# Optimization experiments

Hardware: AMD Instinct MI355X
Metric: run time of the kernel (lower is better)

Reference implementation:

```python
import jax, jax.numpy as jnp
import numpy as np

DIM = 1024
HEADS = 16
HEAD_DIM = DIM // HEADS
B, NQ, NK = 2, 2048, 2048


def setup_inputs() -> dict:
    key = jax.random.key(0)
    ks = jax.random.split(key, 8)
    s = 1.0 / np.sqrt(DIM)
    return {
        "query": jax.random.normal(ks[0], (B, NQ, DIM), jnp.float32),
        "key": jax.random.normal(ks[1], (B, NK, DIM), jnp.float32),
        "value": jax.random.normal(ks[2], (B, NK, DIM), jnp.float32),
        "qpos": jnp.zeros((B, NQ), jnp.int32),
        "kpos": jnp.zeros((B, NK), jnp.int32),
        "Wq": jax.random.normal(ks[3], (DIM, DIM), jnp.float32) * s,
        "Wk": jax.random.normal(ks[4], (DIM, DIM), jnp.float32) * s,
        "Wv": jax.random.normal(ks[5], (DIM, DIM), jnp.float32) * s,
        "Wo": jax.random.normal(ks[6], (DIM, DIM), jnp.float32) * s,
        "bo": jax.random.normal(ks[7], (DIM,), jnp.float32) * s,
    }


def reference(query, key, value, qpos, kpos, Wq, Wk, Wv, Wo, bo):
    # torch nn.Linear: y = x @ W.T (qkv_bias=False)
    Bq, Nq, C = query.shape
    Nk = key.shape[1]
    scale = HEAD_DIM ** -0.5
    # project and split heads: (B, H, N, Dh)
    q = (query @ Wq.T).reshape(Bq, Nq, HEADS, HEAD_DIM).transpose(0, 2, 1, 3)
    k = (key @ Wk.T).reshape(Bq, Nk, HEADS, HEAD_DIM).transpose(0, 2, 1, 3)
    v = (value @ Wv.T).reshape(Bq, Nk, HEADS, HEAD_DIM).transpose(0, 2, 1, 3)
    # rope is None, qk_norm False -> plain softmax attention
    attn = jnp.einsum("bhqd,bhkd->bhqk", q, k) * scale  # [B,H,Nq,Nk]
    attn = jax.nn.softmax(attn, axis=-1)
    x = jnp.einsum("bhqk,bhkd->bhqd", attn, v)
    x = x.transpose(0, 2, 1, 3).reshape(Bq, Nq, C)
    return x @ Wo.T + bo
```

## Files before the change

### kernel.cpp

```cpp
#include <hip/hip_runtime.h>
#include <hip/hip_bf16.h>
#include <stdint.h>

typedef __bf16 bf16_t;
typedef __bf16 bf16x4 __attribute__((ext_vector_type(4)));
typedef __bf16 bf16x8 __attribute__((ext_vector_type(8)));
typedef float  f32x4  __attribute__((ext_vector_type(4)));
typedef unsigned u32x2 __attribute__((ext_vector_type(2)));

#define MFMA16(a,b,c) __builtin_amdgcn_mfma_f32_16x16x32_bf16((a),(b),(c),0,0,0)

static constexpr int DIM = 1024, HEADS = 16, HD = 64, NB = 2, NQ = 2048, NKK = 2048;
static constexpr int MROWS = NB * NQ;
static constexpr float SCALE_Q = 0.18033688011112042f;

__global__ void cvt_w(const float* __restrict__ wq, const float* __restrict__ wk,
                      const float* __restrict__ wv, const float* __restrict__ wo,
                      bf16_t* wqb, bf16_t* wkb, bf16_t* wvb, bf16_t* wob) {
  const int t = blockIdx.y;
  const float* src = t == 0 ? wq : t == 1 ? wk : t == 2 ? wv : wo;
  bf16_t* dst = t == 0 ? wqb : t == 1 ? wkb : t == 2 ? wvb : wob;
  size_t i = (size_t)blockIdx.x * 256 + threadIdx.x;
  float4 val = reinterpret_cast<const float4*>(src)[i];
  bf16x4 o;
  o[0] = (bf16_t)val.x; o[1] = (bf16_t)val.y; o[2] = (bf16_t)val.z; o[3] = (bf16_t)val.w;
  *reinterpret_cast<bf16x4*>(dst + i * 4) = o;
}

template<int ROWS, int TPB = 256>
__device__ __forceinline__ void stage_swz(const bf16_t* gbase, int gstride, bf16_t* lds, int tid) {
#pragma unroll
  for (int c = 0; c < ROWS * 8 / TPB; ++c) {
    int p = c * TPB + tid;
    int r = p >> 3, x = p & 7;
    const bf16_t* src = gbase + (size_t)r * gstride + ((x ^ (r & 7)) << 3);
    __builtin_amdgcn_global_load_lds(
        (const __attribute__((address_space(1))) void*)src,
        (__attribute__((address_space(3))) void*)(lds + (p << 3)),
        16, 0, 0);
  }
}

__device__ __forceinline__ void stage_f32(const float* gbase, int gstride, bf16_t* lds, int tid) {
#pragma unroll
  for (int c = 0; c < 4; ++c) {
    int p = c * 256 + tid;
    int r = p >> 3, x = p & 7;
    const float* src = gbase + (size_t)r * gstride + ((x ^ (r & 7)) << 3);
    float4 a = *reinterpret_cast<const float4*>(src);
    float4 b2 = *reinterpret_cast<const float4*>(src + 4);
    bf16x8 o;
    o[0] = (bf16_t)a.x;  o[1] = (bf16_t)a.y;  o[2] = (bf16_t)a.z;  o[3] = (bf16_t)a.w;
    o[4] = (bf16_t)b2.x; o[5] = (bf16_t)b2.y; o[6] = (bf16_t)b2.z; o[7] = (bf16_t)b2.w;
    *reinterpret_cast<bf16x8*>(lds + (p << 3)) = o;
  }
}

__device__ __forceinline__ bf16x8 lds_read8_swz(const bf16_t* lds, int row, int chunk) {
  int sc = chunk ^ (row & 7);
  return *reinterpret_cast<const bf16x8*>(lds + row * 64 + (sc << 3));
}

__device__ __forceinline__ unsigned cvtpk_bf16(float lo, float hi) {
  unsigned r;
  asm("v_cvt_pk_bf16_f32 %0, %1, %2" : "=v"(r) : "v"(lo), "v"(hi));
  return r;
}

__global__ __launch_bounds__(256) void gemm_qkv(const float* __restrict__ qf32,
                                                const float* __restrict__ kf32,
                                                const float* __restrict__ vf32,
                                                const bf16_t* __restrict__ Wq,
                                                const bf16_t* __restrict__ Wk,
                                                const bf16_t* __restrict__ Wv,
                                                bf16_t* __restrict__ Qp,
                                                bf16_t* __restrict__ Kp,
                                                bf16_t* __restrict__ Vt) {
  constexpr int K = DIM, N = DIM;
  __shared__ __align__(16) bf16_t As[128 * 64];
  __shared__ __align__(16) bf16_t Bs[128 * 64];
  const int tid = threadIdx.x;
  const int lane = tid & 63, wid = tid >> 6;
  const int l15 = lane & 15, lg = lane >> 4;
  const int wr = wid >> 1, wc = wid & 1;

  int d = blockIdx.x + 24 * blockIdx.y;
  int j = d & 7, rest = d >> 3;
  int m_ = rest & 7, gq = rest >> 3;
  int g = 8 * gq + j;
  const int bm = g / 3, sel = g % 3, bnl = m_;

  const float*  Af = sel == 0 ? qf32 : sel == 1 ? kf32 : vf32;
  const bf16_t* Bt = sel == 0 ? Wq : sel == 1 ? Wk : Wv;
  const float*  Abase = Af + (size_t)(bm * 128) * K;
  const bf16_t* Bbase = Bt + (size_t)(bnl * 128) * K;

  f32x4 acc[4][4];
#pragma unroll
  for (int m = 0; m < 4; ++m)
#pragma unroll
    for (int n = 0; n < 4; ++n) acc[m][n] = (f32x4){0.f, 0.f, 0.f, 0.f};

  for (int k0 = 0; k0 < K; k0 += 64) {
    __syncthreads();
    stage_f32(Abase + k0, K, As, tid);
    stage_swz<128>(Bbase + k0, K, Bs, tid);
    __syncthreads();
#pragma unroll
    for (int kk = 0; kk < 2; ++kk) {
      bf16x8 af[4], bfr[4];
#pragma unroll
      for (int m = 0; m < 4; ++m) af[m] = lds_read8_swz(As, wr * 64 + m * 16 + l15, kk * 4 + lg);
#pragma unroll
      for (int n = 0; n < 4; ++n) bfr[n] = lds_read8_swz(Bs, wc * 64 + n * 16 + l15, kk * 4 + lg);
#pragma unroll
      for (int m = 0; m < 4; ++m)
#pragma unroll
        for (int n = 0; n < 4; ++n)
          acc[m][n] = MFMA16(af[m], bfr[n], acc[m][n]);
    }
  }

  if (sel == 2) {
#pragma unroll
    for (int m = 0; m < 4; ++m) {
      int row0 = bm * 128 + wr * 64 + m * 16 + lg * 4;
      int bb = row0 >> 11, kv = row0 & 2047;
#pragma unroll
      for (int n = 0; n < 4; ++n) {
        int col = bnl * 128 + wc * 64 + n * 16 + l15;
        int hh = col >> 6, dd = col & 63;
        bf16x4 pk;
#pragma unroll
        for (int jj = 0; jj < 4; ++jj) pk[jj] = (bf16_t)acc[m][n][jj];
        *reinterpret_cast<bf16x4*>(Vt + (((size_t)((bb * 16 + hh) * 64 + dd)) << 11) + kv) = pk;
      }
    }
  } else {
    bf16_t* Cout = sel == 0 ? Qp : Kp;
    const float scale = sel == 0 ? SCALE_Q : 1.0f;
#pragma unroll
    for (int m = 0; m < 4; ++m)
#pragma unroll
      for (int n = 0; n < 4; ++n)
#pragma unroll
        for (int jj = 0; jj < 4; ++jj) {
          int row = bm * 128 + wr * 64 + m * 16 + lg * 4 + jj;
          int col = bnl * 128 + wc * 64 + n * 16 + l15;
          Cout[(size_t)row * N + col] = (bf16_t)(acc[m][n][jj] * scale);
        }
  }
}

__global__ __launch_bounds__(256) void gemm_out(const bf16_t* __restrict__ A,
                                                const bf16_t* __restrict__ Bt,
                                                float* __restrict__ Cout,
                                                const float* __restrict__ bias) {
  constexpr int K = DIM, N = DIM;
  __shared__ __align__(16) bf16_t As[128 * 64];
  __shared__ __align__(16) bf16_t Bs[128 * 64];
  const int tid = threadIdx.x;
  const int lane = tid & 63, wid = tid >> 6;
  const int l15 = lane & 15, lg = lane >> 4;
  const int wr = wid >> 1, wc = wid & 1;
  const int bn = blockIdx.x, bm = blockIdx.y;

  const bf16_t* Abase = A + (size_t)(bm * 128) * K;
  const bf16_t* Bbase = Bt + (size_t)(bn * 128) * K;

  f32x4 acc[4][4];
#pragma unroll
  for (int m = 0; m < 4; ++m)
#pragma unroll
    for (int n = 0; n < 4; ++n) acc[m][n] = (f32x4){0.f, 0.f, 0.f, 0.f};

  for (int k0 = 0; k0 < K; k0 += 64) {
    __syncthreads();
    stage_swz<128>(Abase + k0, K, As, tid);
    stage_swz<128>(Bbase + k0, K, Bs, tid);
    __syncthreads();
#pragma unroll
    for (int kk = 0; kk < 2; ++kk) {
      bf16x8 af[4], bfr[4];
#pragma unroll
      for (int m = 0; m < 4; ++m) af[m] = lds_read8_swz(As, wr * 64 + m * 16 + l15, kk * 4 + lg);
#pragma unroll
      for (int n = 0; n < 4; ++n) bfr[n] = lds_read8_swz(Bs, wc * 64 + n * 16 + l15, kk * 4 + lg);
#pragma unroll
      for (int m = 0; m < 4; ++m)
#pragma unroll
        for (int n = 0; n < 4; ++n)
          acc[m][n] = MFMA16(af[m], bfr[n], acc[m][n]);
    }
  }

#pragma unroll
  for (int m = 0; m < 4; ++m)
#pragma unroll
    for (int n = 0; n < 4; ++n)
#pragma unroll
      for (int j = 0; j < 4; ++j) {
        int row = bm * 128 + wr * 64 + m * 16 + lg * 4 + j;
        int col = bn * 128 + wc * 64 + n * 16 + l15;
        Cout[(size_t)row * N + col] = acc[m][n][j] + bias[col];
      }
}

__global__ __launch_bounds__(512) void attn_fused(const bf16_t* __restrict__ Qp,
                                                  const bf16_t* __restrict__ Kp,
                                                  const bf16_t* __restrict__ Vt,
                                                  bf16_t* __restrict__ Xa) {
  __shared__ __align__(16) bf16_t Ks[4][64 * 64];
  __shared__ __align__(16) bf16_t Vs[4][64 * 64];
  __shared__ __align__(16) bf16_t Ps[8][16 * 64];
  const int tid = threadIdx.x;
  const int lane = tid & 63, wid = tid >> 6;
  const int l15 = lane & 15, lg = lane >> 4;
  const int rot = (l15 & 7) * 8;

  int id = blockIdx.x + 16 * (blockIdx.y + 16 * blockIdx.z);
  int swz = (id & 7) * 64 + (id >> 3);
  const int bx = swz & 15, h = (swz >> 4) & 15, b = swz >> 8;
  const int q0 = bx * 128;

  const bf16_t* qbase = Qp + ((size_t)(b * NQ + q0)) * DIM + h * HD;
  const bf16_t* kbase = Kp + ((size_t)b * NKK) * DIM + h * HD;
  const bf16_t* vbase = Vt + ((size_t)((b * HEADS + h) * HD)) * NKK;

  stage_swz<128, 512>(qbase, DIM, &Ks[0][0], tid);
  __syncthreads();
  bf16x8 qf[2];
  qf[0] = lds_read8_swz(&Ks[0][0], wid * 16 + l15, lg);
  qf[1] = lds_read8_swz(&Ks[0][0], wid * 16 + l15, 4 + lg);
  __syncthreads();

  float m_ = -1e30f, l_ = 0.f;
  f32x4 o[4];
#pragma unroll
  for (int n = 0; n < 4; ++n) o[n] = (f32x4){0.f, 0.f, 0.f, 0.f};

  constexpr int NT = NKK / 64;

  stage_swz<64, 512>(kbase, DIM, &Ks[0][0], tid);
  stage_swz<64, 512>(vbase, NKK, &Vs[0][0], tid);
  stage_swz<64, 512>(kbase + (size_t)64 * DIM, DIM, &Ks[1][0], tid);
  stage_swz<64, 512>(vbase + 64, NKK, &Vs[1][0], tid);

  for (int t = 0; t < NT; t += 2) {
    if (t + 2 < NT) {
      stage_swz<64, 512>(kbase + (size_t)(t + 2) * 64 * DIM, DIM, &Ks[(t + 2) & 3][0], tid);
      stage_swz<64, 512>(vbase + (t + 2) * 64, NKK, &Vs[(t + 2) & 3][0], tid);
      stage_swz<64, 512>(kbase + (size_t)(t + 3) * 64 * DIM, DIM, &Ks[(t + 3) & 3][0], tid);
      stage_swz<64, 512>(vbase + (t + 3) * 64, NKK, &Vs[(t + 3) & 3][0], tid);
      asm volatile("s_waitcnt vmcnt(4)" ::: "memory");
    } else {
      asm volatile("s_waitcnt vmcnt(0)" ::: "memory");
    }
    __builtin_amdgcn_s_barrier();
    __builtin_amdgcn_sched_barrier(0);

#pragma unroll
    for (int u = 0; u < 2; ++u) {
      const int j = t + u;
      const bf16_t* kl = &Ks[j & 3][0];
      const bf16_t* vl = &Vs[j & 3][0];

      f32x4 scur[4];
      __builtin_amdgcn_s_setprio(1);
#pragma unroll
      for (int tt = 0; tt < 4; ++tt) {
        bf16x8 kf0 = lds_read8_swz(kl, tt * 16 + l15, lg);
        bf16x8 kf1 = lds_read8_swz(kl, tt * 16 + l15, 4 + lg);
        f32x4 a = (f32x4){0.f, 0.f, 0.f, 0.f};
        a = MFMA16(kf0, qf[0], a);
        a = MFMA16(kf1, qf[1], a);
        scur[tt] = a;
      }
      __builtin_amdgcn_s_setprio(0);

      float rm = scur[0][0];
#pragma unroll
      for (int tt = 0; tt < 4; ++tt)
#pragma unroll
        for (int jj = 0; jj < 4; ++jj) rm = fmaxf(rm, scur[tt][jj]);
      rm = fmaxf(rm, __shfl_xor(rm, 16));
      rm = fmaxf(rm, __shfl_xor(rm, 32));
      if (!__all(rm <= m_ + 8.f)) {
        float mn = fmaxf(m_, rm);
        float al = exp2f(m_ - mn);
        m_ = mn;
        l_ *= al;
#pragma unroll
        for (int n = 0; n < 4; ++n)
#pragma unroll
          for (int jj = 0; jj < 4; ++jj) o[n][jj] *= al;
      }
      float rs = 0.f;
#pragma unroll
      for (int tt = 0; tt < 4; ++tt)
#pragma unroll
        for (int jj = 0; jj < 4; ++jj) {
          float p = exp2f(scur[tt][jj] - m_);
          scur[tt][jj] = p;
          rs += p;
        }
      rs += __shfl_xor(rs, 16);
      rs += __shfl_xor(rs, 32);
      l_ += rs;

      bf16_t* Pw = &Ps[wid][0];
#pragma unroll
      for (int tt = 0; tt < 4; ++tt) {
        unsigned w0 = cvtpk_bf16(scur[tt][0], scur[tt][1]);
        unsigned w1 = cvtpk_bf16(scur[tt][2], scur[tt][3]);
        int col = (16 * tt + 4 * lg + rot) & 63;
        u32x2 pk2 = {w0, w1};
        *reinterpret_cast<u32x2*>(reinterpret_cast<char*>(Pw) + l15 * 128 + col * 2) = pk2;
      }
      asm volatile("s_waitcnt lgkmcnt(0)" ::: "memory");
      bf16x8 pf[2];
#pragma unroll
      for (int kt = 0; kt < 2; ++kt) {
        int col = (32 * kt + 8 * lg + rot) & 63;
        pf[kt] = *reinterpret_cast<const bf16x8*>(reinterpret_cast<const char*>(Pw) + l15 * 128 + col * 2);
      }

      __builtin_amdgcn_s_setprio(1);
#pragma unroll
      for (int n = 0; n < 4; ++n) {
#pragma unroll
        for (int kt = 0; kt < 2; ++kt) {
          bf16x8 vf = lds_read8_swz(vl, n * 16 + l15, 4 * kt + lg);
          o[n] = MFMA16(vf, pf[kt], o[n]);
        }
      }
      __builtin_amdgcn_s_setprio(0);
    }

    __builtin_amdgcn_s_barrier();
    __builtin_amdgcn_sched_barrier(0);
  }

  float inv = 1.f / l_;
  int q = q0 + wid * 16 + l15;
  bf16_t* ob = Xa + ((size_t)(b * NQ + q)) * DIM + h * HD;
#pragma unroll
  for (int n = 0; n < 4; ++n) {
    bf16x4 pk;
#pragma unroll
    for (int j = 0; j < 4; ++j) pk[j] = (bf16_t)(o[n][j] * inv);
    *reinterpret_cast<bf16x4*>(ob + n * 16 + 4 * lg) = pk;
  }
}

extern "C" void kernel_launch(void* const* d_in, const int* in_sizes, int n_in,
                              void* d_out, int out_size, void* d_ws, size_t ws_size,
                              hipStream_t stream) {
  (void)in_sizes; (void)n_in; (void)out_size; (void)ws_size;
  const float* q  = (const float*)d_in[0];
  const float* k  = (const float*)d_in[1];
  const float* v  = (const float*)d_in[2];
  const float* Wq = (const float*)d_in[5];
  const float* Wk = (const float*)d_in[6];
  const float* Wv = (const float*)d_in[7];
  const float* Wo = (const float*)d_in[8];
  const float* bo = (const float*)d_in[9];
  float* out = (float*)d_out;

  bf16_t* ws = (bf16_t*)d_ws;
  const size_t SZ_IN = (size_t)MROWS * DIM;
  const size_t SZ_W  = (size_t)DIM * DIM;
  bf16_t* qb  = ws;
  bf16_t* kb  = qb  + SZ_IN;
  bf16_t* vb  = kb  + SZ_IN;
  bf16_t* wqb = vb  + SZ_IN;
  bf16_t* wkb = wqb + SZ_W;
  bf16_t* wvb = wkb + SZ_W;
  bf16_t* wob = wvb + SZ_W;
  bf16_t* Qp  = wob + SZ_W;
  bf16_t* Kp  = Qp  + SZ_IN;
  bf16_t* Vtp = Kp  + SZ_IN;
  bf16_t* Xa  = qb;

  cvt_w<<<dim3(1024, 4), 256, 0, stream>>>(Wq, Wk, Wv, Wo, wqb, wkb, wvb, wob);

  gemm_qkv<<<dim3(24, MROWS / 128), 256, 0, stream>>>(q, k, v, wqb, wkb, wvb,
                                                      Qp, Kp, Vtp);

  attn_fused<<<dim3(NQ / 128, HEADS, NB), 512, 0, stream>>>(Qp, Kp, Vtp, Xa);

  gemm_out<<<dim3(DIM / 128, MROWS / 128), 256, 0, stream>>>(Xa, wob, out, bo);
}
```

Measured before the change: 151.6 us.

## Software-pipeline QKV GEMM with register-prefetched A and double-buffered B tiles

Restructures the QKV projection GEMM main loop so the next K-tile's fp32 A data is loaded into registers and its bf16 B tile is staged asynchronously into a second LDS buffer while the current tile is being computed. The loop is manually unrolled by two with even and odd register sets, and uses raw s_barrier plus sched_barrier instead of __syncthreads. The aim is to hide global-memory latency behind MFMA work. In exchange it adds LDS for the second B buffer and extra registers for the prefetched A rows, which may reduce occupancy. It also relies on implicit vmcnt ordering for B readiness.

Result: slower. 160.5 us (+5.9%).

```diff
diff --git a/kernel.cpp b/kernel.cpp
--- a/kernel.cpp
+++ b/kernel.cpp
@@ -41,14 +41,21 @@
   }
 }
 
-__device__ __forceinline__ void stage_f32(const float* gbase, int gstride, bf16_t* lds, int tid) {
+__device__ __forceinline__ void loadA_f32(const float* gbase, int tid, float4* r) {
 #pragma unroll
   for (int c = 0; c < 4; ++c) {
     int p = c * 256 + tid;
-    int r = p >> 3, x = p & 7;
-    const float* src = gbase + (size_t)r * gstride + ((x ^ (r & 7)) << 3);
-    float4 a = *reinterpret_cast<const float4*>(src);
-    float4 b2 = *reinterpret_cast<const float4*>(src + 4);
+    int rr = p >> 3, x = p & 7;
+    const float* src = gbase + (size_t)rr * DIM + ((x ^ (rr & 7)) << 3);
+    r[2 * c]     = *reinterpret_cast<const float4*>(src);
+    r[2 * c + 1] = *reinterpret_cast<const float4*>(src + 4);
+  }
+}
+__device__ __forceinline__ void writeA(bf16_t* lds, int tid, const float4* r) {
+#pragma unroll
+  for (int c = 0; c < 4; ++c) {
+    int p = c * 256 + tid;
+    float4 a = r[2 * c], b2 = r[2 * c + 1];
     bf16x8 o;
     o[0] = (bf16_t)a.x;  o[1] = (bf16_t)a.y;  o[2] = (bf16_t)a.z;  o[3] = (bf16_t)a.w;
     o[4] = (bf16_t)b2.x; o[5] = (bf16_t)b2.y; o[6] = (bf16_t)b2.z; o[7] = (bf16_t)b2.w;
@@ -76,9 +83,9 @@
                                                 bf16_t* __restrict__ Qp,
                                                 bf16_t* __restrict__ Kp,
                                                 bf16_t* __restrict__ Vt) {
-  constexpr int K = DIM, N = DIM;
+  constexpr int K = DIM, N = DIM, NKI = K / 64;
   __shared__ __align__(16) bf16_t As[128 * 64];
-  __shared__ __align__(16) bf16_t Bs[128 * 64];
+  __shared__ __align__(16) bf16_t Bs[2][128 * 64];
   const int tid = threadIdx.x;
   const int lane = tid & 63, wid = tid >> 6;
   const int l15 = lane & 15, lg = lane >> 4;
@@ -101,25 +108,59 @@
 #pragma unroll
     for (int n = 0; n < 4; ++n) acc[m][n] = (f32x4){0.f, 0.f, 0.f, 0.f};
 
-  for (int k0 = 0; k0 < K; k0 += 64) {
-    __syncthreads();
-    stage_f32(Abase + k0, K, As, tid);
-    stage_swz<128>(Bbase + k0, K, Bs, tid);
-    __syncthreads();
-#pragma unroll
-    for (int kk = 0; kk < 2; ++kk) {
-      bf16x8 af[4], bfr[4];
-#pragma unroll
-      for (int m = 0; m < 4; ++m) af[m] = lds_read8_swz(As, wr * 64 + m * 16 + l15, kk * 4 + lg);
-#pragma unroll
-      for (int n = 0; n < 4; ++n) bfr[n] = lds_read8_swz(Bs, wc * 64 + n * 16 + l15, kk * 4 + lg);
-#pragma unroll
-      for (int m = 0; m < 4; ++m)
-#pragma unroll
-        for (int n = 0; n < 4; ++n)
-          acc[m][n] = MFMA16(af[m], bfr[n], acc[m][n]);
-    }
-  }
+  float4 rE[8], rO[8];
+
+#define QKV_COMPUTE(BSEL)                                                      \
+  do {                                                                         \
+    _Pragma("unroll")                                                          \
+    for (int kk = 0; kk < 2; ++kk) {                                           \
+      bf16x8 af[4], bfr[4];                                                    \
+      _Pragma("unroll")                                                        \
+      for (int m = 0; m < 4; ++m)                                              \
+        af[m] = lds_read8_swz(As, wr * 64 + m * 16 + l15, kk * 4 + lg);        \
+      _Pragma("unroll")                                                        \
+      for (int n = 0; n < 4; ++n)                                              \
+        bfr[n] = lds_read8_swz(&Bs[BSEL][0], wc * 64 + n * 16 + l15, kk * 4 + lg); \
+      _Pragma("unroll")                                                        \
+      for (int m = 0; m < 4; ++m)                                              \
+        _Pragma("unroll")                                                      \
+        for (int n = 0; n < 4; ++n)                                            \
+          acc[m][n] = MFMA16(af[m], bfr[n], acc[m][n]);                        \
+    }                                                                          \
+  } while (0)
+
+  stage_swz<128>(Bbase, K, &Bs[0][0], tid);
+  loadA_f32(Abase, tid, rE);
+
+#pragma unroll 1
+  for (int t = 0; t < NKI; t += 2) {
+    __builtin_amdgcn_s_barrier();
+    __builtin_amdgcn_sched_barrier(0);
+    if (t + 1 < NKI) {
+      stage_swz<128>(Bbase + (t + 1) * 64, K, &Bs[(t + 1) & 1][0], tid);
+      loadA_f32(Abase + (t + 1) * 64, tid, rO);
+    }
+    writeA(As, tid, rE);
+    asm volatile("s_waitcnt lgkmcnt(0)" ::: "memory");
+    __builtin_amdgcn_s_barrier();
+    __builtin_amdgcn_sched_barrier(0);
+    QKV_COMPUTE(t & 1);
+
+    if (t + 1 < NKI) {
+      __builtin_amdgcn_s_barrier();
+      __builtin_amdgcn_sched_barrier(0);
+      if (t + 2 < NKI) {
+        stage_swz<128>(Bbase + (t + 2) * 64, K, &Bs[t & 1][0], tid);
+        loadA_f32(Abase + (t + 2) * 64, tid, rE);
+      }
+      writeA(As, tid, rO);
+      asm volatile("s_waitcnt lgkmcnt(0)" ::: "memory");
+      __builtin_amdgcn_s_barrier();
+      __builtin_amdgcn_sched_barrier(0);
+      QKV_COMPUTE((t + 1) & 1);
+    }
+  }
+#undef QKV_COMPUTE
 
   if (sel == 2) {
 #pragma unroll
```

## Process two 16-row query groups per wave in fused attention

Applied to the files above, without the earlier changes.

Each wave now handles 32 query rows, as two groups, instead of 16, and each block covers 256 queries instead of 128. K and V fragments are read from LDS once per tile and reused across both groups' MFMAs. The aim is to halve LDS reads and global K/V staging per query. In exchange the grid is halved to 256 blocks, and LDS and register use per block grow, so occupancy and latency hiding drop.

New measurement: 162.6 us. 1.07x slower.

```diff
diff --git a/kernel.cpp b/kernel.cpp
--- a/kernel.cpp
+++ b/kernel.cpp
@@ -212,32 +212,37 @@
                                                   bf16_t* __restrict__ Xa) {
   __shared__ __align__(16) bf16_t Ks[4][64 * 64];
   __shared__ __align__(16) bf16_t Vs[4][64 * 64];
-  __shared__ __align__(16) bf16_t Ps[8][16 * 64];
+  __shared__ __align__(16) bf16_t Ps[8][32 * 64];
   const int tid = threadIdx.x;
   const int lane = tid & 63, wid = tid >> 6;
   const int l15 = lane & 15, lg = lane >> 4;
   const int rot = (l15 & 7) * 8;
 
-  int id = blockIdx.x + 16 * (blockIdx.y + 16 * blockIdx.z);
-  int swz = (id & 7) * 64 + (id >> 3);
-  const int bx = swz & 15, h = (swz >> 4) & 15, b = swz >> 8;
-  const int q0 = bx * 128;
+  int id = blockIdx.x + 8 * (blockIdx.y + 16 * blockIdx.z);
+  int swz = (id & 7) * 32 + (id >> 3);
+  const int bx = swz & 7, h = (swz >> 3) & 15, b = swz >> 7;
+  const int q0 = bx * 256;
 
   const bf16_t* qbase = Qp + ((size_t)(b * NQ + q0)) * DIM + h * HD;
   const bf16_t* kbase = Kp + ((size_t)b * NKK) * DIM + h * HD;
   const bf16_t* vbase = Vt + ((size_t)((b * HEADS + h) * HD)) * NKK;
 
-  stage_swz<128, 512>(qbase, DIM, &Ks[0][0], tid);
+  stage_swz<256, 512>(qbase, DIM, &Ks[0][0], tid);
   __syncthreads();
-  bf16x8 qf[2];
-  qf[0] = lds_read8_swz(&Ks[0][0], wid * 16 + l15, lg);
-  qf[1] = lds_read8_swz(&Ks[0][0], wid * 16 + l15, 4 + lg);
+  bf16x8 qf[2][2];
+#pragma unroll
+  for (int g = 0; g < 2; ++g) {
+    qf[g][0] = lds_read8_swz(&Ks[0][0], wid * 32 + g * 16 + l15, lg);
+    qf[g][1] = lds_read8_swz(&Ks[0][0], wid * 32 + g * 16 + l15, 4 + lg);
+  }
   __syncthreads();
 
-  float m_ = -1e30f, l_ = 0.f;
-  f32x4 o[4];
-#pragma unroll
-  for (int n = 0; n < 4; ++n) o[n] = (f32x4){0.f, 0.f, 0.f, 0.f};
+  float m_[2] = {-1e30f, -1e30f}, l_[2] = {0.f, 0.f};
+  f32x4 o[2][4];
+#pragma unroll
+  for (int g = 0; g < 2; ++g)
+#pragma unroll
+    for (int n = 0; n < 4; ++n) o[g][n] = (f32x4){0.f, 0.f, 0.f, 0.f};
 
   constexpr int NT = NKK / 64;
 
@@ -265,91 +270,113 @@
       const bf16_t* kl = &Ks[j & 3][0];
       const bf16_t* vl = &Vs[j & 3][0];
 
-      f32x4 scur[4];
+      bf16x8 kf0[4], kf1[4];
+#pragma unroll
+      for (int tt = 0; tt < 4; ++tt) {
+        kf0[tt] = lds_read8_swz(kl, tt * 16 + l15, lg);
+        kf1[tt] = lds_read8_swz(kl, tt * 16 + l15, 4 + lg);
+      }
+
+      f32x4 s[2][4];
+#pragma unroll
+      for (int g = 0; g < 2; ++g)
+#pragma unroll
+        for (int tt = 0; tt < 4; ++tt) s[g][tt] = (f32x4){0.f, 0.f, 0.f, 0.f};
       __builtin_amdgcn_s_setprio(1);
 #pragma unroll
-      for (int tt = 0; tt < 4; ++tt) {
-        bf16x8 kf0 = lds_read8_swz(kl, tt * 16 + l15, lg);
-        bf16x8 kf1 = lds_read8_swz(kl, tt * 16 + l15, 4 + lg);
-        f32x4 a = (f32x4){0.f, 0.f, 0.f, 0.f};
-        a = MFMA16(kf0, qf[0], a);
-        a = MFMA16(kf1, qf[1], a);
-        scur[tt] = a;
+      for (int g = 0; g < 2; ++g)
+#pragma unroll
+        for (int tt = 0; tt < 4; ++tt) {
+          s[g][tt] = MFMA16(kf0[tt], qf[g][0], s[g][tt]);
+          s[g][tt] = MFMA16(kf1[tt], qf[g][1], s[g][tt]);
+        }
+      __builtin_amdgcn_s_setprio(0);
+
+#pragma unroll
+      for (int g = 0; g < 2; ++g) {
+        float rm = s[g][0][0];
+#pragma unroll
+        for (int tt = 0; tt < 4; ++tt)
+#pragma unroll
+          for (int jj = 0; jj < 4; ++jj) rm = fmaxf(rm, s[g][tt][jj]);
+        rm = fmaxf(rm, __shfl_xor(rm, 16));
+        rm = fmaxf(rm, __shfl_xor(rm, 32));
+        if (!__all(rm <= m_[g] + 8.f)) {
+          float mn = fmaxf(m_[g], rm);
+          float al = exp2f(m_[g] - mn);
+          m_[g] = mn;
+          l_[g] *= al;
+#pragma unroll
+          for (int n = 0; n < 4; ++n)
+#pragma unroll
+            for (int jj = 0; jj < 4; ++jj) o[g][n][jj] *= al;
+        }
+        float rs = 0.f;
+#pragma unroll
+        for (int tt = 0; tt < 4; ++tt)
+#pragma unroll
+          for (int jj = 0; jj < 4; ++jj) {
+            float p = exp2f(s[g][tt][jj] - m_[g]);
+            s[g][tt][jj] = p;
+            rs += p;
+          }
+        rs += __shfl_xor(rs, 16);
+        rs += __shfl_xor(rs, 32);
+        l_[g] += rs;
+      }
+
+      bf16_t* Pw = &Ps[wid][0];
+#pragma unroll
+      for (int g = 0; g < 2; ++g)
+#pragma unroll
+        for (int tt = 0; tt < 4; ++tt) {
+          unsigned w0 = cvtpk_bf16(s[g][tt][0], s[g][tt][1]);
+          unsigned w1 = cvtpk_bf16(s[g][tt][2], s[g][tt][3]);
+          int col = (16 * tt + 4 * lg + rot) & 63;
+          u32x2 pk2 = {w0, w1};
+          *reinterpret_cast<u32x2*>(reinterpret_cast<char*>(Pw) + (g * 16 + l15) * 128 + col * 2) = pk2;
+        }
+      asm volatile("s_waitcnt lgkmcnt(0)" ::: "memory");
+      bf16x8 pf[2][2];
+#pragma unroll
+      for (int g = 0; g < 2; ++g)
+#pragma unroll
+        for (int kt = 0; kt < 2; ++kt) {
+          int col = (32 * kt + 8 * lg + rot) & 63;
+          pf[g][kt] = *reinterpret_cast<const bf16x8*>(
+              reinterpret_cast<const char*>(Pw) + (g * 16 + l15) * 128 + col * 2);
+        }
+
+      __builtin_amdgcn_s_setprio(1);
+#pragma unroll
+      for (int n = 0; n < 4; ++n) {
+        bf16x8 vf0 = lds_read8_swz(vl, n * 16 + l15, lg);
+        bf16x8 vf1 = lds_read8_swz(vl, n * 16 + l15, 4 + lg);
+#pragma unroll
+        for (int g = 0; g < 2; ++g) {
+          o[g][n] = MFMA16(vf0, pf[g][0], o[g][n]);
+          o[g][n] = MFMA16(vf1, pf[g][1], o[g][n]);
+        }
       }
       __builtin_amdgcn_s_setprio(0);
-
-      float rm = scur[0][0];
-#pragma unroll
-      for (int tt = 0; tt < 4; ++tt)
-#pragma unroll
-        for (int jj = 0; jj < 4; ++jj) rm = fmaxf(rm, scur[tt][jj]);
-      rm = fmaxf(rm, __shfl_xor(rm, 16));
-      rm = fmaxf(rm, __shfl_xor(rm, 32));
-      if (!__all(rm <= m_ + 8.f)) {
-        float mn = fmaxf(m_, rm);
-        float al = exp2f(m_ - mn);
-        m_ = mn;
-        l_ *= al;
-#pragma unroll
-        for (int n = 0; n < 4; ++n)
-#pragma unroll
-          for (int jj = 0; jj < 4; ++jj) o[n][jj] *= al;
-      }
-      float rs = 0.f;
-#pragma unroll
-      for (int tt = 0; tt < 4; ++tt)
-#pragma unroll
-        for (int jj = 0; jj < 4; ++jj) {
-          float p = exp2f(scur[tt][jj] - m_);
-          scur[tt][jj] = p;
-          rs += p;
-        }
-      rs += __shfl_xor(rs, 16);
-      rs += __shfl_xor(rs, 32);
-      l_ += rs;
-
-      bf16_t* Pw = &Ps[wid][0];
-#pragma unroll
-      for (int tt = 0; tt < 4; ++tt) {
-        unsigned w0 = cvtpk_bf16(scur[tt][0], scur[tt][1]);
-        unsigned w1 = cvtpk_bf16(scur[tt][2], scur[tt][3]);
-        int col = (16 * tt + 4 * lg + rot) & 63;
-        u32x2 pk2 = {w0, w1};
-        *reinterpret_cast<u32x2*>(reinterpret_cast<char*>(Pw) + l15 * 128 + col * 2) = pk2;
-      }
-      asm volatile("s_waitcnt lgkmcnt(0)" ::: "memory");
-      bf16x8 pf[2];
-#pragma unroll
-      for (int kt = 0; kt < 2; ++kt) {
-        int col = (32 * kt + 8 * lg + rot) & 63;
-        pf[kt] = *reinterpret_cast<const bf16x8*>(reinterpret_cast<const char*>(Pw) + l15 * 128 + col * 2);
-      }
-
-      __builtin_amdgcn_s_setprio(1);
-#pragma unroll
-      for (int n = 0; n < 4; ++n) {
-#pragma unroll
-        for (int kt = 0; kt < 2; ++kt) {
-          bf16x8 vf = lds_read8_swz(vl, n * 16 + l15, 4 * kt + lg);
-          o[n] = MFMA16(vf, pf[kt], o[n]);
-        }
-      }
-      __builtin_amdgcn_s_setprio(0);
     }
 
     __builtin_amdgcn_s_barrier();
     __builtin_amdgcn_sched_barrier(0);
   }
 
-  float inv = 1.f / l_;
-  int q = q0 + wid * 16 + l15;
-  bf16_t* ob = Xa + ((size_t)(b * NQ + q)) * DIM + h * HD;
-#pragma unroll
-  for (int n = 0; n < 4; ++n) {
-    bf16x4 pk;
-#pragma unroll
-    for (int j = 0; j < 4; ++j) pk[j] = (bf16_t)(o[n][j] * inv);
-    *reinterpret_cast<bf16x4*>(ob + n * 16 + 4 * lg) = pk;
+#pragma unroll
+  for (int g = 0; g < 2; ++g) {
+    float inv = 1.f / l_[g];
+    int q = q0 + wid * 32 + g * 16 + l15;
+    bf16_t* ob = Xa + ((size_t)(b * NQ + q)) * DIM + h * HD;
+#pragma unroll
+    for (int n = 0; n < 4; ++n) {
+      bf16x4 pk;
+#pragma unroll
+      for (int j = 0; j < 4; ++j) pk[j] = (bf16_t)(o[g][n][j] * inv);
+      *reinterpret_cast<bf16x4*>(ob + n * 16 + 4 * lg) = pk;
+    }
   }
 }
 
@@ -387,7 +414,7 @@
   gemm_qkv<<<dim3(24, MROWS / 128), 256, 0, stream>>>(q, k, v, wqb, wkb, wvb,
                                                       Qp, Kp, Vtp);
 
-  attn_fused<<<dim3(NQ / 128, HEADS, NB), 512, 0, stream>>>(Qp, Kp, Vtp, Xa);
+  attn_fused<<<dim3(NQ / 256, HEADS, NB), 512, 0, stream>>>(Qp, Kp, Vtp, Xa);
 
   gemm_out<<<dim3(DIM / 128, MROWS / 128), 256, 0, stream>>>(Xa, wob, out, bo);
 }
```

## Software-pipeline QKV GEMM with register-prefetched A and double-buffered B tiles

Applied to the files above, without the earlier changes.

Restructures the QKV projection GEMM main loop so the next K-slice is fetched while the current one is computed. The fp32 A tile is prefetched into registers and converted to bf16 when written to LDS. The B weight tile is double-buffered in LDS through global_load_lds. Each iteration now has one prefetch-then-compute phase with explicit barriers instead of load-sync-compute, to hide global memory latency. It adds register pressure (eight float4 per thread) and an extra LDS buffer, and it relies on the implicit vmcnt ordering of the A register loads to ensure the async B tile has landed.

Result: faster. 145.9 us (-3.8%).

```diff
diff --git a/kernel.cpp b/kernel.cpp
--- a/kernel.cpp
+++ b/kernel.cpp
@@ -41,14 +41,21 @@
   }
 }
 
-__device__ __forceinline__ void stage_f32(const float* gbase, int gstride, bf16_t* lds, int tid) {
+__device__ __forceinline__ void loadA_f32(const float* gbase, int tid, float4* r) {
 #pragma unroll
   for (int c = 0; c < 4; ++c) {
     int p = c * 256 + tid;
-    int r = p >> 3, x = p & 7;
-    const float* src = gbase + (size_t)r * gstride + ((x ^ (r & 7)) << 3);
-    float4 a = *reinterpret_cast<const float4*>(src);
-    float4 b2 = *reinterpret_cast<const float4*>(src + 4);
+    int rr = p >> 3, x = p & 7;
+    const float* src = gbase + (size_t)rr * DIM + ((x ^ (rr & 7)) << 3);
+    r[2 * c]     = *reinterpret_cast<const float4*>(src);
+    r[2 * c + 1] = *reinterpret_cast<const float4*>(src + 4);
+  }
+}
+__device__ __forceinline__ void writeA(bf16_t* lds, int tid, const float4* r) {
+#pragma unroll
+  for (int c = 0; c < 4; ++c) {
+    int p = c * 256 + tid;
+    float4 a = r[2 * c], b2 = r[2 * c + 1];
     bf16x8 o;
     o[0] = (bf16_t)a.x;  o[1] = (bf16_t)a.y;  o[2] = (bf16_t)a.z;  o[3] = (bf16_t)a.w;
     o[4] = (bf16_t)b2.x; o[5] = (bf16_t)b2.y; o[6] = (bf16_t)b2.z; o[7] = (bf16_t)b2.w;
@@ -76,9 +83,9 @@
                                                 bf16_t* __restrict__ Qp,
                                                 bf16_t* __restrict__ Kp,
                                                 bf16_t* __restrict__ Vt) {
-  constexpr int K = DIM, N = DIM;
+  constexpr int K = DIM, N = DIM, NKI = K / 64;
   __shared__ __align__(16) bf16_t As[128 * 64];
-  __shared__ __align__(16) bf16_t Bs[128 * 64];
+  __shared__ __align__(16) bf16_t Bs[2][128 * 64];
   const int tid = threadIdx.x;
   const int lane = tid & 63, wid = tid >> 6;
   const int l15 = lane & 15, lg = lane >> 4;
@@ -101,18 +108,31 @@
 #pragma unroll
     for (int n = 0; n < 4; ++n) acc[m][n] = (f32x4){0.f, 0.f, 0.f, 0.f};
 
-  for (int k0 = 0; k0 < K; k0 += 64) {
-    __syncthreads();
-    stage_f32(Abase + k0, K, As, tid);
-    stage_swz<128>(Bbase + k0, K, Bs, tid);
-    __syncthreads();
+  float4 rA[8];
+
+  stage_swz<128>(Bbase, K, &Bs[0][0], tid);
+  loadA_f32(Abase, tid, rA);
+
+#pragma unroll 1
+  for (int t = 0; t < NKI; ++t) {
+    __builtin_amdgcn_s_barrier();
+    __builtin_amdgcn_sched_barrier(0);
+    if (t + 1 < NKI)
+      stage_swz<128>(Bbase + (t + 1) * 64, K, &Bs[(t + 1) & 1][0], tid);
+    writeA(As, tid, rA);
+    if (t + 1 < NKI)
+      loadA_f32(Abase + (t + 1) * 64, tid, rA);
+    asm volatile("s_waitcnt lgkmcnt(0)" ::: "memory");
+    __builtin_amdgcn_sched_barrier(0);
+    __builtin_amdgcn_s_barrier();
+    __builtin_amdgcn_sched_barrier(0);
 #pragma unroll
     for (int kk = 0; kk < 2; ++kk) {
       bf16x8 af[4], bfr[4];
 #pragma unroll
       for (int m = 0; m < 4; ++m) af[m] = lds_read8_swz(As, wr * 64 + m * 16 + l15, kk * 4 + lg);
 #pragma unroll
-      for (int n = 0; n < 4; ++n) bfr[n] = lds_read8_swz(Bs, wc * 64 + n * 16 + l15, kk * 4 + lg);
+      for (int n = 0; n < 4; ++n) bfr[n] = lds_read8_swz(&Bs[t & 1][0], wc * 64 + n * 16 + l15, kk * 4 + lg);
 #pragma unroll
       for (int m = 0; m < 4; ++m)
 #pragma unroll
```
